# Optimization experiments

Measured on AMD Instinct MI355X. Metric: run time of the kernel, lower is better.

Reference implementation:

```python
import jax, jax.numpy as jnp
import numpy as np

NS = 16          # scalar (0e) multiplicity
NV = 4           # vector (1o) multiplicity
NG = 50          # gaussian smearing basis size
GS_STOP = 5.0
HID = 64
WNUM = (NS + NV) * NS + (NS + NV) * NV  # 400
SQRT3 = float(np.sqrt(3.0))


def gaussian_smearing(dist):
    # GaussianSmearing(start=0, stop=5, num_gaussians=50)
    offset = jnp.linspace(0.0, GS_STOP, NG)
    step = GS_STOP / (NG - 1)
    coeff = -0.5 / (step * step)
    d = dist[:, None] - offset[None, :] + 1e-6
    return jnp.exp(coeff * d * d)


def setup_inputs() -> dict:
    key = jax.random.key(0)
    ks = jax.random.split(key, 6)
    N, E = 10000, 320000
    in_dim = NG + 2 * NS  # 82
    node_attr = jax.random.normal(ks[0], (N, NS + 3 * NV), dtype=jnp.float32)
    pos = jax.random.normal(ks[1], (N, 3), dtype=jnp.float32) * 10.0
    edge_index = jax.random.randint(ks[2], (2, E), 0, N, dtype=jnp.int64)
    W1 = jax.random.normal(ks[3], (in_dim, HID), dtype=jnp.float32) / np.sqrt(in_dim)
    b1 = jnp.zeros((HID,), jnp.float32)
    W2 = jax.random.normal(ks[4], (HID, WNUM), dtype=jnp.float32) / np.sqrt(HID)
    b2 = jnp.zeros((WNUM,), jnp.float32)
    return {"node_attr": node_attr, "pos": pos, "W1": W1, "b1": b1,
            "W2": W2, "b2": b2, "edge_index": edge_index}


def reference(node_attr, pos, W1, b1, W2, b2, edge_index):
    N = node_attr.shape[0]
    src, dst = edge_index[0], edge_index[1]
    E = src.shape[0]

    # --- build_cg: edge vectors, gaussian edge attr, 1st-order spherical harmonics ---
    edge_vec = pos[dst] - pos[src]                       # [E,3]
    dist = jnp.linalg.norm(edge_vec, axis=-1)            # [E]
    edge_attr = gaussian_smearing(dist)                  # [E,NG]
    unit = edge_vec / jnp.maximum(dist, 1e-8)[:, None]
    sh_0e = jnp.ones((E,), node_attr.dtype)              # Y_0 (component norm)
    # e3nn l=1 ordering (y, z, x), component normalization => sqrt(3)*unit
    sh_1o = SQRT3 * jnp.stack([unit[:, 1], unit[:, 2], unit[:, 0]], axis=-1)

    # --- get_edge_attr + edge MLP producing per-edge TP weights ---
    ef = jnp.concatenate([edge_attr, node_attr[src, :NS], node_attr[dst, :NS]], axis=-1)
    w = jax.nn.relu(ef @ W1 + b1) @ W2 + b2              # [E, WNUM]
    n0e = (NS + NV) * NS
    w_0e = w[:, :n0e].reshape(E, NS + NV, NS) / np.sqrt(NS + NV)
    w_1o = w[:, n0e:].reshape(E, NS + NV, NV) / np.sqrt(NS + NV)

    in_0e = node_attr[src, :NS]                          # [E,NS]
    in_1o = node_attr[src, NS:].reshape(E, NV, 3)        # [E,NV,3]
    # 0e outputs: 0e*0e and 1o.1o/sqrt(3)
    o0 = jnp.concatenate([in_0e * sh_0e[:, None],
                          (in_1o * sh_1o[:, None, :]).sum(-1) / SQRT3], axis=-1)  # [E,NS+NV]
    out_0e = jnp.einsum('ei,eio->eo', o0, w_0e)          # [E,NS]
    # 1o outputs: 0e x 1o and 1o x 0e
    o1 = jnp.concatenate([in_0e[:, :, None] * sh_1o[:, None, :],
                          in_1o * sh_0e[:, None, None]], axis=1)                  # [E,NS+NV,3]
    out_1o = jnp.einsum('eic,eio->eoc', o1, w_1o).reshape(E, 3 * NV)              # [E,3*NV]
    msg = jnp.concatenate([out_0e, out_1o], axis=-1)     # [E, NS+3*NV]

    # --- scatter mean to destination nodes + residual ---
    agg = jax.ops.segment_sum(msg, dst, num_segments=N)
    cnt = jax.ops.segment_sum(jnp.ones((E,), msg.dtype), dst, num_segments=N)
    agg = agg / jnp.maximum(cnt, 1.0)[:, None]
    return node_attr + agg
```

## Files before the change

kernel.cpp:

```cpp
#include <hip/hip_runtime.h>
#include <math.h>

typedef _Float16 half8 __attribute__((ext_vector_type(8)));
typedef float f32x4 __attribute__((ext_vector_type(4)));
typedef unsigned int u32x4 __attribute__((ext_vector_type(4)));
typedef unsigned int u32x2 __attribute__((ext_vector_type(2)));

namespace {
constexpr int kNS = 16;
constexpr int kNV = 4;
constexpr int kNG = 50;
constexpr int kHID = 64;
constexpr int kAttr = 28;
constexpr int kWNUM = 400;
constexpr float kStep = 5.0f / 49.0f;
constexpr float kCoeff = -0.5f / (kStep * kStep);
constexpr float kSqrt3 = 1.7320508075688772f;
constexpr float kInvSqrt3 = 0.57735026918962576f;
constexpr float kInvSqrt20 = 0.22360679774997896f;
constexpr int kRowB = 208;
constexpr int kImg1Bytes = 96 * 64 * 2;
constexpr int kImg2Bytes = 64 * 400 * 2;
}

__device__ __forceinline__ unsigned short f2h(float x) {
  _Float16 h = (_Float16)x;
  unsigned short r;
  __builtin_memcpy(&r, &h, 2);
  return r;
}
__device__ __forceinline__ unsigned pack2(float lo, float hi) {
  return (unsigned)f2h(lo) | ((unsigned)f2h(hi) << 16);
}

__global__ __launch_bounds__(256) void init_kernel(
    const float* __restrict__ W1, const float* __restrict__ W2,
    const float* __restrict__ node_attr,
    unsigned short* __restrict__ img1, unsigned short* __restrict__ img2,
    int* __restrict__ cnt, float* __restrict__ agg, int aggN4, int N) {
  const int gtid = blockIdx.x * 256 + threadIdx.x;
  const int gsz = gridDim.x * 256;
  f32x4* agg4 = (f32x4*)agg;
  const f32x4* na4 = (const f32x4*)node_attr;
  for (int i = gtid; i < aggN4; i += gsz) agg4[i] = na4[i];
  for (int i = gtid; i < N; i += gsz) cnt[i] = 0;
  for (int i = gtid; i < 96 * 64 + 64 * 400; i += gsz) {
    if (i < 96 * 64) {
      const int m = i >> 6, n = i & 63;
      float v = 0.0f;
      if (m < 50) v = W1[m * 64 + n];
      else if (m >= 56 && m < 88) v = W1[(m - 6) * 64 + n];
      img1[((m >> 3) * 64 + n) * 8 + (m & 7)] = f2h(v);
    } else {
      const int j = i - 96 * 64;
      const int m = j / 400, n = j % 400;
      img2[((m >> 3) * 400 + n) * 8 + (m & 7)] = f2h(W2[m * 400 + n]);
    }
  }
}

__global__ __launch_bounds__(256) void hist_rank_kernel(
    const int* __restrict__ edge_index, int* __restrict__ cnt,
    int* __restrict__ rank, int E) {
  const int e = blockIdx.x * blockDim.x + threadIdx.x;
  if (e >= E) return;
  rank[e] = atomicAdd(cnt + edge_index[E + e], 1);
}

__global__ __launch_bounds__(256) void scan_kernel(
    const int* __restrict__ cnt, int* __restrict__ node_start, int N) {
  __shared__ int wsum[4];
  const int tid = threadIdx.x;
  const int lane = tid & 63;
  const int wv = tid >> 6;
  const int n4 = (N + 3) >> 2;
  const int tiles = (n4 + 255) / 256;
  int running = 0;
  for (int k = 0; k < tiles; ++k) {
    const int i4 = k * 256 + tid;
    int4 v = {0, 0, 0, 0};
    const int base = i4 * 4;
    if (i4 < n4) {
      if (base + 3 < N) {
        v = *(const int4*)(cnt + base);
      } else {
        if (base + 0 < N) v.x = cnt[base + 0];
        if (base + 1 < N) v.y = cnt[base + 1];
        if (base + 2 < N) v.z = cnt[base + 2];
      }
    }
    const int e1 = v.x, e2 = v.x + v.y, e3 = e2 + v.z, s4 = e3 + v.w;
    int incl = s4;
#pragma unroll
    for (int d = 1; d < 64; d <<= 1) {
      const int y = __shfl_up(incl, d);
      if (lane >= d) incl += y;
    }
    if (lane == 63) wsum[wv] = incl;
    __syncthreads();
    int wbase = 0;
#pragma unroll
    for (int w = 0; w < 4; ++w) wbase += (w < wv) ? wsum[w] : 0;
    const int block_total = wsum[0] + wsum[1] + wsum[2] + wsum[3];
    const int tbase = running + wbase + (incl - s4);
    if (i4 < n4) {
      if (base + 0 < N) node_start[base + 0] = tbase;
      if (base + 1 < N) node_start[base + 1] = tbase + e1;
      if (base + 2 < N) node_start[base + 2] = tbase + e2;
      if (base + 3 < N) node_start[base + 3] = tbase + e3;
    }
    running += block_total;
    __syncthreads();
  }
}

__global__ __launch_bounds__(256) void scatter_kernel(
    const int* __restrict__ edge_index, const int* __restrict__ node_start,
    const int* __restrict__ rank, int2* __restrict__ sedge, int E) {
  const int e = blockIdx.x * blockDim.x + threadIdx.x;
  if (e >= E) return;
  const int s = edge_index[e];
  const int d = edge_index[E + e];
  sedge[node_start[d] + rank[e]] = int2{s, d};
}

__global__ __launch_bounds__(256, 3) void tfn_mfma_kernel(
    const float* __restrict__ node_attr, const float* __restrict__ pos,
    const float* __restrict__ b1, const float* __restrict__ b2,
    const char* __restrict__ img1, const char* __restrict__ img2,
    const int2* __restrict__ sedge, const int* __restrict__ cnt,
    float* __restrict__ agg, int E) {
  __shared__ __align__(16) char ub[256 * kRowB];

  const int tid = threadIdx.x;
  const int t = blockIdx.x * 256 + tid;
  const int lane = tid & 63;
  const int wv = tid >> 6;
  const int lc = lane & 15, lq = lane >> 4;

  const bool valid = (t < E);
  int src = 0, dstv = -1;
  if (valid) {
    const int2 se = sedge[t];
    src = se.x;
    dstv = se.y;
  }
  const int dn = valid ? dstv : 0;

  const float psx = pos[src * 3 + 0], psy = pos[src * 3 + 1], psz = pos[src * 3 + 2];
  const float pdx = pos[dn * 3 + 0], pdy = pos[dn * 3 + 1], pdz = pos[dn * 3 + 2];
  const float vx = pdx - psx, vy = pdy - psy, vz = pdz - psz;
  const float dist = sqrtf(vx * vx + vy * vy + vz * vz);
  const float rinv = 1.0f / fmaxf(dist, 1e-8f);
  const float sh0 = kSqrt3 * (vy * rinv);
  const float sh1 = kSqrt3 * (vz * rinv);
  const float sh2 = kSqrt3 * (vx * rinv);

  const float* nas = node_attr + (size_t)src * kAttr;
  const float* nad = node_attr + (size_t)dn * kAttr;
  const float4 sa = *(const float4*)(nas + 0);
  const float4 sb = *(const float4*)(nas + 4);
  const float4 sc4 = *(const float4*)(nas + 8);
  const float4 sd4 = *(const float4*)(nas + 12);
  const float4 va = *(const float4*)(nas + 16);
  const float4 vb = *(const float4*)(nas + 20);
  const float4 vc = *(const float4*)(nas + 24);
  const float4 da = *(const float4*)(nad + 0);
  const float4 db = *(const float4*)(nad + 4);
  const float4 dc4 = *(const float4*)(nad + 8);
  const float4 dd4 = *(const float4*)(nad + 12);

  char* myrow = ub + tid * kRowB;

  {
    const float base = dist + 1e-6f;
#pragma unroll
    for (int c = 0; c < 6; ++c) {
      unsigned p[4];
#pragma unroll
      for (int u = 0; u < 4; ++u) {
        const int k = c * 8 + u * 2;
        const float d0 = base - (float)k * kStep;
        const float d1 = base - (float)(k + 1) * kStep;
        p[u] = pack2(__expf(kCoeff * d0 * d0), __expf(kCoeff * d1 * d1));
      }
      *(u32x4*)(myrow + c * 16) = u32x4{p[0], p[1], p[2], p[3]};
    }
    const float d0 = base - 48.0f * kStep, d1 = base - 49.0f * kStep;
    *(u32x4*)(myrow + 6 * 16) =
        u32x4{pack2(__expf(kCoeff * d0 * d0), __expf(kCoeff * d1 * d1)), 0u, 0u, 0u};
    *(u32x4*)(myrow + 7 * 16) =
        u32x4{pack2(sa.x, sa.y), pack2(sa.z, sa.w), pack2(sb.x, sb.y), pack2(sb.z, sb.w)};
    *(u32x4*)(myrow + 8 * 16) =
        u32x4{pack2(sc4.x, sc4.y), pack2(sc4.z, sc4.w), pack2(sd4.x, sd4.y), pack2(sd4.z, sd4.w)};
    *(u32x4*)(myrow + 9 * 16) =
        u32x4{pack2(da.x, da.y), pack2(da.z, da.w), pack2(db.x, db.y), pack2(db.z, db.w)};
    *(u32x4*)(myrow + 10 * 16) =
        u32x4{pack2(dc4.x, dc4.y), pack2(dc4.z, dc4.w), pack2(dd4.x, dd4.y), pack2(dd4.z, dd4.w)};
    *(u32x4*)(myrow + 11 * 16) = u32x4{0u, 0u, 0u, 0u};
  }

  const float v1f[12] = {va.x, va.y, va.z, va.w, vb.x, vb.y, vb.z, vb.w,
                         vc.x, vc.y, vc.z, vc.w};

  half8 eff[4][3];
#pragma unroll
  for (int g = 0; g < 4; ++g) {
    const char* rp = ub + (wv * 64 + g * 16 + lc) * kRowB;
#pragma unroll
    for (int ks = 0; ks < 3; ++ks)
      eff[g][ks] = *(const half8*)(rp + (ks * 4 + lq) * 16);
  }

  *(f32x4*)(myrow + 8 * 16) = f32x4{sh0, sh1, sh2, v1f[0]};
  *(f32x4*)(myrow + 9 * 16) = f32x4{v1f[1], v1f[2], v1f[3], v1f[4]};
  *(f32x4*)(myrow + 10 * 16) = f32x4{v1f[5], v1f[6], v1f[7], v1f[8]};
  *(f32x4*)(myrow + 11 * 16) = f32x4{v1f[9], v1f[10], v1f[11], 0.0f};

#pragma unroll
  for (int nt = 0; nt < 4; ++nt) {
    const half8 a0 = *(const half8*)(img1 + ((0 + lq) * 64 + nt * 16 + lc) * 16);
    const half8 a1 = *(const half8*)(img1 + ((4 + lq) * 64 + nt * 16 + lc) * 16);
    const half8 a2 = *(const half8*)(img1 + ((8 + lq) * 64 + nt * 16 + lc) * 16);
    const f32x4 bias = *(const f32x4*)(b1 + nt * 16 + lq * 4);
#pragma unroll
    for (int g = 0; g < 4; ++g) {
      f32x4 acc = bias;
      acc = __builtin_amdgcn_mfma_f32_16x16x32_f16(a0, eff[g][0], acc, 0, 0, 0);
      acc = __builtin_amdgcn_mfma_f32_16x16x32_f16(a1, eff[g][1], acc, 0, 0, 0);
      acc = __builtin_amdgcn_mfma_f32_16x16x32_f16(a2, eff[g][2], acc, 0, 0, 0);
      const unsigned p0 = pack2(fmaxf(acc[0], 0.0f), fmaxf(acc[1], 0.0f));
      const unsigned p1 = pack2(fmaxf(acc[2], 0.0f), fmaxf(acc[3], 0.0f));
      const int row = wv * 64 + g * 16 + lc;
      *(u32x2*)(ub + row * kRowB + nt * 32 + lq * 8) = u32x2{p0, p1};
    }
  }

  half8 hf[4][2];
#pragma unroll
  for (int g = 0; g < 4; ++g) {
    const char* rp = ub + (wv * 64 + g * 16 + lc) * kRowB;
    hf[g][0] = *(const half8*)(rp + (0 + lq) * 16);
    hf[g][1] = *(const half8*)(rp + (4 + lq) * 16);
  }

  float shv[4][3], v1h[4][3];
#pragma unroll
  for (int g = 0; g < 4; ++g) {
    const char* rp = ub + (wv * 64 + g * 16 + lc) * kRowB;
#pragma unroll
    for (int c = 0; c < 3; ++c) {
      shv[g][c] = *(const float*)(rp + 128 + 4 * c);
      v1h[g][c] = *(const float*)(rp + 140 + 12 * lq + 4 * c);
    }
  }

  {
    const float t0 = (v1f[0] * sh0 + v1f[1] * sh1 + v1f[2] * sh2) * kInvSqrt3;
    const float t1 = (v1f[3] * sh0 + v1f[4] * sh1 + v1f[5] * sh2) * kInvSqrt3;
    const float t2 = (v1f[6] * sh0 + v1f[7] * sh1 + v1f[8] * sh2) * kInvSqrt3;
    const float t3 = (v1f[9] * sh0 + v1f[10] * sh1 + v1f[11] * sh2) * kInvSqrt3;
    *(f32x4*)(myrow + 0) = f32x4{sa.x, sa.y, sa.z, sa.w};
    *(f32x4*)(myrow + 16) = f32x4{sb.x, sb.y, sb.z, sb.w};
    *(f32x4*)(myrow + 32) = f32x4{sc4.x, sc4.y, sc4.z, sc4.w};
    *(f32x4*)(myrow + 48) = f32x4{sd4.x, sd4.y, sd4.z, sd4.w};
    *(f32x4*)(myrow + 64) = f32x4{t0, t1, t2, t3};
  }

  float macc0[4][4] = {};
  float macc1[4][4][3] = {};

#pragma unroll 5
  for (int nt = 0; nt < 20; ++nt) {
    const half8 w0 = *(const half8*)(img2 + ((0 + lq) * 400 + nt * 16 + lc) * 16);
    const half8 w1 = *(const half8*)(img2 + ((4 + lq) * 400 + nt * 16 + lc) * 16);
    const f32x4 bias = *(const f32x4*)(b2 + nt * 16 + lq * 4);
#pragma unroll
    for (int g = 0; g < 4; ++g) {
      f32x4 acc = bias;
      acc = __builtin_amdgcn_mfma_f32_16x16x32_f16(w0, hf[g][0], acc, 0, 0, 0);
      acc = __builtin_amdgcn_mfma_f32_16x16x32_f16(w1, hf[g][1], acc, 0, 0, 0);
      const char* rp0 = ub + (wv * 64 + g * 16 + lc) * kRowB;
      const float o0v = *(const float*)(rp0 + 4 * nt);
#pragma unroll
      for (int r = 0; r < 4; ++r) macc0[g][r] = fmaf(o0v, acc[r], macc0[g][r]);
    }
  }
#pragma unroll
  for (int nt = 20; nt < 24; ++nt) {
    const half8 w0 = *(const half8*)(img2 + ((0 + lq) * 400 + nt * 16 + lc) * 16);
    const half8 w1 = *(const half8*)(img2 + ((4 + lq) * 400 + nt * 16 + lc) * 16);
    const f32x4 bias = *(const f32x4*)(b2 + nt * 16 + lq * 4);
#pragma unroll
    for (int g = 0; g < 4; ++g) {
      f32x4 acc = bias;
      acc = __builtin_amdgcn_mfma_f32_16x16x32_f16(w0, hf[g][0], acc, 0, 0, 0);
      acc = __builtin_amdgcn_mfma_f32_16x16x32_f16(w1, hf[g][1], acc, 0, 0, 0);
      const char* rp0 = ub + (wv * 64 + g * 16 + lc) * kRowB;
      const float ssv = *(const float*)(rp0 + 16 * (nt - 20) + 4 * lq);
      float pc[3];
#pragma unroll
      for (int c = 0; c < 3; ++c) pc[c] = ssv * shv[g][c];
#pragma unroll
      for (int r = 0; r < 4; ++r)
#pragma unroll
        for (int c = 0; c < 3; ++c)
          macc1[g][r][c] = fmaf(pc[c], acc[r], macc1[g][r][c]);
    }
  }
  {
    const int nt = 24;
    const half8 w0 = *(const half8*)(img2 + ((0 + lq) * 400 + nt * 16 + lc) * 16);
    const half8 w1 = *(const half8*)(img2 + ((4 + lq) * 400 + nt * 16 + lc) * 16);
    const f32x4 bias = *(const f32x4*)(b2 + nt * 16 + lq * 4);
#pragma unroll
    for (int g = 0; g < 4; ++g) {
      f32x4 acc = bias;
      acc = __builtin_amdgcn_mfma_f32_16x16x32_f16(w0, hf[g][0], acc, 0, 0, 0);
      acc = __builtin_amdgcn_mfma_f32_16x16x32_f16(w1, hf[g][1], acc, 0, 0, 0);
#pragma unroll
      for (int r = 0; r < 4; ++r)
#pragma unroll
        for (int c = 0; c < 3; ++c)
          macc1[g][r][c] = fmaf(v1h[g][c], acc[r], macc1[g][r][c]);
    }
  }

#pragma unroll
  for (int g = 0; g < 4; ++g)
#pragma unroll
    for (int r = 0; r < 4; ++r)
#pragma unroll
      for (int c = 0; c < 3; ++c) {
        float x = macc1[g][r][c];
        x += __shfl_xor(x, 16);
        x += __shfl_xor(x, 32);
        macc1[g][r][c] = x * kInvSqrt20;
      }
#pragma unroll
  for (int g = 0; g < 4; ++g) {
    char* rp = ub + (wv * 64 + g * 16 + lc) * kRowB;
    *(f32x4*)(rp + lq * 16) =
        f32x4{macc0[g][0] * kInvSqrt20, macc0[g][1] * kInvSqrt20,
              macc0[g][2] * kInvSqrt20, macc0[g][3] * kInvSqrt20};
    f32x4 m1;
    if (lq == 1)
      m1 = f32x4{macc1[g][0][0], macc1[g][0][1], macc1[g][0][2], macc1[g][1][0]};
    else if (lq == 2)
      m1 = f32x4{macc1[g][1][1], macc1[g][1][2], macc1[g][2][0], macc1[g][2][1]};
    else
      m1 = f32x4{macc1[g][2][2], macc1[g][3][0], macc1[g][3][1], macc1[g][3][2]};
    if (lq != 0) *(f32x4*)(rp + 48 + lq * 16) = m1;
  }

  float msg[28];
  {
    const char* rp = ub + tid * kRowB;
#pragma unroll
    for (int c = 0; c < 7; ++c) {
      const f32x4 v = *(const f32x4*)(rp + c * 16);
      msg[c * 4 + 0] = v[0];
      msg[c * 4 + 1] = v[1];
      msg[c * 4 + 2] = v[2];
      msg[c * 4 + 3] = v[3];
    }
  }
#pragma unroll
  for (int d = 1; d < 64; d <<= 1) {
    const int od = __shfl_down(dstv, d);
    const bool same = (lane + d < 64) && (od == dstv);
#pragma unroll
    for (int j = 0; j < 28; j++) {
      const float ov = __shfl_down(msg[j], d);
      if (same) msg[j] += ov;
    }
  }
  const int pd = __shfl_up(dstv, 1);
  if ((lane == 0 || pd != dstv) && dstv >= 0) {
    const float rc = 1.0f / fmaxf((float)cnt[dstv], 1.0f);
    float* ap = agg + (size_t)dstv * kAttr;
#pragma unroll
    for (int j = 0; j < 28; j++) atomicAdd(ap + j, msg[j] * rc);
  }
}

extern "C" void kernel_launch(void* const* d_in, const int* in_sizes, int n_in,
                              void* d_out, int out_size, void* d_ws, size_t ws_size,
                              hipStream_t stream) {
  const float* node_attr = (const float*)d_in[0];
  const float* pos = (const float*)d_in[1];
  const float* W1 = (const float*)d_in[2];
  const float* b1 = (const float*)d_in[3];
  const float* W2 = (const float*)d_in[4];
  const float* b2 = (const float*)d_in[5];
  const int* edge_index = (const int*)d_in[6];

  const int N = in_sizes[0] / kAttr;
  const int E = in_sizes[6] / 2;

  char* wsc = (char*)d_ws;
  unsigned short* img1 = (unsigned short*)wsc;
  unsigned short* img2 = (unsigned short*)(wsc + kImg1Bytes);
  int* cnt = (int*)(wsc + kImg1Bytes + kImg2Bytes);
  int* node_start = cnt + N;
  int* rank = node_start + N;
  int2* sedge = (int2*)(rank + E);

  float* agg = (float*)d_out;
  const int aggN4 = out_size / 4;
  const int eblocks = (E + 255) / 256;

  init_kernel<<<512, 256, 0, stream>>>(W1, W2, node_attr, img1, img2, cnt, agg,
                                       aggN4, N);
  hist_rank_kernel<<<eblocks, 256, 0, stream>>>(edge_index, cnt, rank, E);
  scan_kernel<<<1, 256, 0, stream>>>(cnt, node_start, N);
  scatter_kernel<<<eblocks, 256, 0, stream>>>(edge_index, node_start, rank,
                                              sedge, E);
  tfn_mfma_kernel<<<eblocks, 256, 0, stream>>>(
      node_attr, pos, b1, b2, (const char*)img1, (const char*)img2,
      sedge, cnt, agg, E);
}
```

Before: 107.6 us.

## Pack segmented-reduction messages into fp16 pairs and vectorize LDS reads

The per-wave segmented reduction now shuffles messages as packed half2 values, which halves the number of cross-lane shuffles (14 instead of 28 per step). The LDS layout for sh and vector inputs is padded to 16-byte rows so they can be read as single vector loads. The per-edge scalar o0 values in the first weight loop are loaded four at a time instead of one per tile. Summing messages in fp16 lowers accumulation precision and risks overflow or tolerance failures.

```diff
diff --git a/kernel.cpp b/kernel.cpp
--- a/kernel.cpp
+++ b/kernel.cpp
@@ -2,6 +2,7 @@
 #include <math.h>
 
 typedef _Float16 half8 __attribute__((ext_vector_type(8)));
+typedef _Float16 h2 __attribute__((ext_vector_type(2)));
 typedef float f32x4 __attribute__((ext_vector_type(4)));
 typedef unsigned int u32x4 __attribute__((ext_vector_type(4)));
 typedef unsigned int u32x2 __attribute__((ext_vector_type(2)));
@@ -212,10 +213,11 @@
       eff[g][ks] = *(const half8*)(rp + (ks * 4 + lq) * 16);
   }
 
-  *(f32x4*)(myrow + 8 * 16) = f32x4{sh0, sh1, sh2, v1f[0]};
-  *(f32x4*)(myrow + 9 * 16) = f32x4{v1f[1], v1f[2], v1f[3], v1f[4]};
-  *(f32x4*)(myrow + 10 * 16) = f32x4{v1f[5], v1f[6], v1f[7], v1f[8]};
-  *(f32x4*)(myrow + 11 * 16) = f32x4{v1f[9], v1f[10], v1f[11], 0.0f};
+  *(f32x4*)(myrow + 8 * 16) = f32x4{sh0, sh1, sh2, 0.0f};
+  *(f32x4*)(myrow + 9 * 16) = f32x4{v1f[0], v1f[1], v1f[2], 0.0f};
+  *(f32x4*)(myrow + 10 * 16) = f32x4{v1f[3], v1f[4], v1f[5], 0.0f};
+  *(f32x4*)(myrow + 11 * 16) = f32x4{v1f[6], v1f[7], v1f[8], 0.0f};
+  *(f32x4*)(myrow + 12 * 16) = f32x4{v1f[9], v1f[10], v1f[11], 0.0f};
 
 #pragma unroll
   for (int nt = 0; nt < 4; ++nt) {
@@ -248,11 +250,10 @@
 #pragma unroll
   for (int g = 0; g < 4; ++g) {
     const char* rp = ub + (wv * 64 + g * 16 + lc) * kRowB;
-#pragma unroll
-    for (int c = 0; c < 3; ++c) {
-      shv[g][c] = *(const float*)(rp + 128 + 4 * c);
-      v1h[g][c] = *(const float*)(rp + 140 + 12 * lq + 4 * c);
-    }
+    const f32x4 s4 = *(const f32x4*)(rp + 128);
+    shv[g][0] = s4[0]; shv[g][1] = s4[1]; shv[g][2] = s4[2];
+    const f32x4 v4 = *(const f32x4*)(rp + 144 + 16 * lq);
+    v1h[g][0] = v4[0]; v1h[g][1] = v4[1]; v1h[g][2] = v4[2];
   }
 
   {
@@ -270,20 +271,27 @@
   float macc0[4][4] = {};
   float macc1[4][4][3] = {};
 
-#pragma unroll 5
-  for (int nt = 0; nt < 20; ++nt) {
-    const half8 w0 = *(const half8*)(img2 + ((0 + lq) * 400 + nt * 16 + lc) * 16);
-    const half8 w1 = *(const half8*)(img2 + ((4 + lq) * 400 + nt * 16 + lc) * 16);
-    const f32x4 bias = *(const f32x4*)(b2 + nt * 16 + lq * 4);
-#pragma unroll
-    for (int g = 0; g < 4; ++g) {
-      f32x4 acc = bias;
-      acc = __builtin_amdgcn_mfma_f32_16x16x32_f16(w0, hf[g][0], acc, 0, 0, 0);
-      acc = __builtin_amdgcn_mfma_f32_16x16x32_f16(w1, hf[g][1], acc, 0, 0, 0);
-      const char* rp0 = ub + (wv * 64 + g * 16 + lc) * kRowB;
-      const float o0v = *(const float*)(rp0 + 4 * nt);
-#pragma unroll
-      for (int r = 0; r < 4; ++r) macc0[g][r] = fmaf(o0v, acc[r], macc0[g][r]);
+#pragma unroll
+  for (int q = 0; q < 5; ++q) {
+    f32x4 o0q[4];
+#pragma unroll
+    for (int g = 0; g < 4; ++g)
+      o0q[g] = *(const f32x4*)(ub + (wv * 64 + g * 16 + lc) * kRowB + 16 * q);
+#pragma unroll
+    for (int r = 0; r < 4; ++r) {
+      const int nt = q * 4 + r;
+      const half8 w0 = *(const half8*)(img2 + ((0 + lq) * 400 + nt * 16 + lc) * 16);
+      const half8 w1 = *(const half8*)(img2 + ((4 + lq) * 400 + nt * 16 + lc) * 16);
+      const f32x4 bias = *(const f32x4*)(b2 + nt * 16 + lq * 4);
+#pragma unroll
+      for (int g = 0; g < 4; ++g) {
+        f32x4 acc = bias;
+        acc = __builtin_amdgcn_mfma_f32_16x16x32_f16(w0, hf[g][0], acc, 0, 0, 0);
+        acc = __builtin_amdgcn_mfma_f32_16x16x32_f16(w1, hf[g][1], acc, 0, 0, 0);
+        const float o0v = o0q[g][r];
+#pragma unroll
+        for (int rr = 0; rr < 4; ++rr) macc0[g][rr] = fmaf(o0v, acc[rr], macc0[g][rr]);
+      }
     }
   }
 #pragma unroll
@@ -353,16 +361,14 @@
     if (lq != 0) *(f32x4*)(rp + 48 + lq * 16) = m1;
   }
 
-  float msg[28];
+  h2 hm[14];
   {
     const char* rp = ub + tid * kRowB;
 #pragma unroll
     for (int c = 0; c < 7; ++c) {
       const f32x4 v = *(const f32x4*)(rp + c * 16);
-      msg[c * 4 + 0] = v[0];
-      msg[c * 4 + 1] = v[1];
-      msg[c * 4 + 2] = v[2];
-      msg[c * 4 + 3] = v[3];
+      hm[c * 2 + 0] = h2{(_Float16)v[0], (_Float16)v[1]};
+      hm[c * 2 + 1] = h2{(_Float16)v[2], (_Float16)v[3]};
     }
   }
 #pragma unroll
@@ -370,9 +376,13 @@
     const int od = __shfl_down(dstv, d);
     const bool same = (lane + d < 64) && (od == dstv);
 #pragma unroll
-    for (int j = 0; j < 28; j++) {
-      const float ov = __shfl_down(msg[j], d);
-      if (same) msg[j] += ov;
+    for (int j = 0; j < 14; j++) {
+      int u;
+      __builtin_memcpy(&u, &hm[j], 4);
+      u = __shfl_down(u, d);
+      h2 o;
+      __builtin_memcpy(&o, &u, 4);
+      if (same) hm[j] += o;
     }
   }
   const int pd = __shfl_up(dstv, 1);
@@ -380,7 +390,10 @@
     const float rc = 1.0f / fmaxf((float)cnt[dstv], 1.0f);
     float* ap = agg + (size_t)dstv * kAttr;
 #pragma unroll
-    for (int j = 0; j < 28; j++) atomicAdd(ap + j, msg[j] * rc);
+    for (int j = 0; j < 14; j++) {
+      atomicAdd(ap + 2 * j + 0, (float)hm[j][0] * rc);
+      atomicAdd(ap + 2 * j + 1, (float)hm[j][1] * rc);
+    }
   }
 }
 
```

Result: slower. 411.9 us (+282.8%).

## Replace per-node atomic scatter with deterministic partial slots and finalize kernel

Applied to the files above, without the earlier changes.

Removes the atomicAdd-based scatter-mean. Because edges are sorted by destination, each wave now writes its segment sums with plain vector stores. A segment that runs across a wave boundary goes to a per-wave overflow slot. A new finalize kernel adds each node's own slot and any overflow slots it spans, divides by the count, and adds the residual. This trades 28 atomics per segment for extra partial-buffer traffic, an extra zeroing pass over a larger buffer, and one more kernel launch.

```diff
diff --git a/kernel.cpp b/kernel.cpp
--- a/kernel.cpp
+++ b/kernel.cpp
@@ -35,14 +35,12 @@
 
 __global__ __launch_bounds__(256) void init_kernel(
     const float* __restrict__ W1, const float* __restrict__ W2,
-    const float* __restrict__ node_attr,
     unsigned short* __restrict__ img1, unsigned short* __restrict__ img2,
-    int* __restrict__ cnt, float* __restrict__ agg, int aggN4, int N) {
+    int* __restrict__ cnt, float* __restrict__ part, int partN4, int N) {
   const int gtid = blockIdx.x * 256 + threadIdx.x;
   const int gsz = gridDim.x * 256;
-  f32x4* agg4 = (f32x4*)agg;
-  const f32x4* na4 = (const f32x4*)node_attr;
-  for (int i = gtid; i < aggN4; i += gsz) agg4[i] = na4[i];
+  f32x4* p4 = (f32x4*)part;
+  for (int i = gtid; i < partN4; i += gsz) p4[i] = f32x4{0.f, 0.f, 0.f, 0.f};
   for (int i = gtid; i < N; i += gsz) cnt[i] = 0;
   for (int i = gtid; i < 96 * 64 + 64 * 400; i += gsz) {
     if (i < 96 * 64) {
@@ -128,8 +126,7 @@
     const float* __restrict__ node_attr, const float* __restrict__ pos,
     const float* __restrict__ b1, const float* __restrict__ b2,
     const char* __restrict__ img1, const char* __restrict__ img2,
-    const int2* __restrict__ sedge, const int* __restrict__ cnt,
-    float* __restrict__ agg, int E) {
+    const int2* __restrict__ sedge, float* __restrict__ part, int N, int E) {
   __shared__ __align__(16) char ub[256 * kRowB];
 
   const int tid = threadIdx.x;
@@ -377,11 +374,29 @@
   }
   const int pd = __shfl_up(dstv, 1);
   if ((lane == 0 || pd != dstv) && dstv >= 0) {
-    const float rc = 1.0f / fmaxf((float)cnt[dstv], 1.0f);
-    float* ap = agg + (size_t)dstv * kAttr;
-#pragma unroll
-    for (int j = 0; j < 28; j++) atomicAdd(ap + j, msg[j] * rc);
-  }
+    const int slot = (lane == 0) ? (N + (t >> 6)) : dstv;
+    float* pp = part + (size_t)slot * kAttr;
+#pragma unroll
+    for (int c = 0; c < 7; ++c)
+      *(f32x4*)(pp + c * 4) =
+          f32x4{msg[c * 4 + 0], msg[c * 4 + 1], msg[c * 4 + 2], msg[c * 4 + 3]};
+  }
+}
+
+__global__ __launch_bounds__(256) void tfn_finalize_kernel(
+    const float* __restrict__ node_attr, const int* __restrict__ cnt,
+    const int* __restrict__ node_start, const float* __restrict__ part,
+    float* __restrict__ out, int N, int total) {
+  const int i = blockIdx.x * blockDim.x + threadIdx.x;
+  if (i >= total) return;
+  const int n = i / kAttr;
+  const int j = i - n * kAttr;
+  const int c = cnt[n];
+  float s = part[(size_t)n * kAttr + j];
+  const int ns = node_start[n];
+  for (int k = (ns + 63) >> 6; k * 64 < ns + c; ++k)
+    s += part[(size_t)(N + k) * kAttr + j];
+  out[i] = node_attr[i] + s / fmaxf((float)c, 1.0f);
 }
 
 extern "C" void kernel_launch(void* const* d_in, const int* in_sizes, int n_in,
@@ -397,6 +412,7 @@
 
   const int N = in_sizes[0] / kAttr;
   const int E = in_sizes[6] / 2;
+  const int nslots = N + (E + 63) / 64;
 
   char* wsc = (char*)d_ws;
   unsigned short* img1 = (unsigned short*)wsc;
@@ -405,18 +421,20 @@
   int* node_start = cnt + N;
   int* rank = node_start + N;
   int2* sedge = (int2*)(rank + E);
-
-  float* agg = (float*)d_out;
-  const int aggN4 = out_size / 4;
+  float* part = (float*)(sedge + E);
+
+  const int partN4 = (nslots * kAttr) / 4;
   const int eblocks = (E + 255) / 256;
-
-  init_kernel<<<512, 256, 0, stream>>>(W1, W2, node_attr, img1, img2, cnt, agg,
-                                       aggN4, N);
+  const int total = N * kAttr;
+
+  init_kernel<<<512, 256, 0, stream>>>(W1, W2, img1, img2, cnt, part, partN4, N);
   hist_rank_kernel<<<eblocks, 256, 0, stream>>>(edge_index, cnt, rank, E);
   scan_kernel<<<1, 256, 0, stream>>>(cnt, node_start, N);
   scatter_kernel<<<eblocks, 256, 0, stream>>>(edge_index, node_start, rank,
                                               sedge, E);
   tfn_mfma_kernel<<<eblocks, 256, 0, stream>>>(
       node_attr, pos, b1, b2, (const char*)img1, (const char*)img2,
-      sedge, cnt, agg, E);
-}
+      sedge, part, N, E);
+  tfn_finalize_kernel<<<(total + 255) / 256, 256, 0, stream>>>(
+      node_attr, cnt, node_start, part, (float*)d_out, N, total);
+}
```

After: 95.25 us. 1.13x faster.
